# Optimization experiments

Measured on AMD Instinct MI355X. Metric: run time of the kernel, lower is better.

Reference implementation:

```python
import jax, jax.numpy as jnp
import numpy as np

NEG_INF = -1e10  # masked_fill value from the torch module


def setup_inputs() -> dict:
    key = jax.random.key(0)
    k1, k2, k3, k4, k5 = jax.random.split(key, 5)
    B, S, H = 64, 2048, 512
    return {
        "decoder_hidden": jax.random.normal(k1, (B, H), dtype=jnp.float32),
        "encoder_outputs": jax.random.normal(k2, (B, S, 2 * H), dtype=jnp.float32),
        "mask": jnp.ones((B, S), dtype=jnp.int32),
        "Wd": jax.random.normal(k3, (H, H), dtype=jnp.float32) * (1.0 / np.sqrt(H)),
        "We": jax.random.normal(k4, (2 * H, H), dtype=jnp.float32) * (1.0 / np.sqrt(2 * H)),
        "v": jax.random.normal(k5, (H,), dtype=jnp.float32) * (1.0 / np.sqrt(H)),
    }


def reference(decoder_hidden, encoder_outputs, mask, Wd, We, v):
    # decoder_proj: (B, H); encoder_proj: (B, S, H)
    dec_proj = decoder_hidden @ Wd
    enc_proj = jnp.einsum("bse,eh->bsh", encoder_outputs, We)
    energy = jnp.tanh(dec_proj[:, None, :] + enc_proj)  # (B, S, H)
    scores = jnp.einsum("bsh,h->bs", energy, v)  # (B, S)
    scores = jnp.where(mask == 0, NEG_INF, scores)
    attn_weights = jax.nn.softmax(scores, axis=1)  # (B, S)
    context = jnp.einsum("bs,bsd->bd", attn_weights, encoder_outputs)  # (B, 2H)
    return (context, attn_weights)
```

## Files before the change

### kernel.cpp

```cpp
#include <hip/hip_runtime.h>

typedef _Float16 f16;
typedef f16  f16x4 __attribute__((ext_vector_type(4)));
typedef f16  f16x8 __attribute__((ext_vector_type(8)));
typedef float f32x4 __attribute__((ext_vector_type(4)));

#define B_  64
#define S_  2048
#define H_  512
#define K_  1024

__device__ __forceinline__ float fast_tanh(float x){
  float ax = fabsf(x);
  float t  = __expf(-2.0f*ax);
  float r  = (1.0f - t) / (1.0f + t);
  return x < 0.0f ? -r : r;
}

__global__ __launch_bounds__(256) void prep_k(const float* __restrict__ We,
                                              f16* __restrict__ Bg,
                                              const float* __restrict__ dh,
                                              const float* __restrict__ Wd,
                                              float* __restrict__ dp,
                                              const float* __restrict__ vvg,
                                              float* __restrict__ vC){
  __shared__ float s_dh[512];
  if (blockIdx.x < 2048){
    int idx = blockIdx.x*256 + threadIdx.x;
    int k = idx >> 9, col = idx & 511;
    Bg[((k>>3)<<12) + (col<<3) + (k&7)] = (f16)We[idx];
  } else if (blockIdx.x < 2176){
    int idx = blockIdx.x - 2048;
    int b = idx >> 1, cg = idx & 1;
    int col = (cg<<8) + threadIdx.x;
    for (int i = threadIdx.x; i < 512; i += 256) s_dh[i] = dh[(b<<9) + i];
    __syncthreads();
    float a0=0.f,a1=0.f,a2=0.f,a3=0.f;
    for (int k = 0; k < 512; k += 4){
      a0 += s_dh[k+0]*Wd[(k+0)*512 + col];
      a1 += s_dh[k+1]*Wd[(k+1)*512 + col];
      a2 += s_dh[k+2]*Wd[(k+2)*512 + col];
      a3 += s_dh[k+3]*Wd[(k+3)*512 + col];
    }
    dp[(b<<9) + col] = (a0+a1)+(a2+a3);
  } else {
    int t = threadIdx.x;
    float a = fabsf(vvg[t]) + fabsf(vvg[t+256]);
    #pragma unroll
    for (int o = 32; o >= 1; o >>= 1) a += __shfl_xor(a, o);
    if ((t & 63) == 0) s_dh[t>>6] = a;
    __syncthreads();
    if (t == 0) vC[0] = s_dh[0]+s_dh[1]+s_dh[2]+s_dh[3];
  }
}

__global__ __launch_bounds__(512, 2) void fused_k(
    const float* __restrict__ enc,
    const f16*   __restrict__ Bg,
    const float* __restrict__ dp,
    const float* __restrict__ vvg,
    const float* __restrict__ vC,
    const int*   __restrict__ mask,
    float*       __restrict__ pbuf,
    float*       __restrict__ denom,
    float*       __restrict__ part)
{
  __shared__ __align__(16) f16 At[2][2048];
  __shared__ __align__(16) f16 Bt[2][16384];
  __shared__ float s_sc[64];

  const int tid  = threadIdx.x;
  const int lane = tid & 63;
  const int wave = tid >> 6;
  const int b    = blockIdx.x >> 5;
  const int s0   = (blockIdx.x & 31) << 6;

  if (tid < 64) s_sc[tid] = 0.0f;

  const int arow = tid >> 3;
  const int akq  = tid & 7;
  const int kgrp = akq >> 1, apar = akq & 1;
  const float* aG = enc + ((size_t)(b*S_ + s0 + arow) << 10) + (akq << 2);
  const int aDst = (kgrp<<9) + ((arow ^ (kgrp<<1))<<3) + (apar<<2);

  const int r16 = lane & 15, g = lane >> 4;
  const int aFrag = (g<<9) + ((r16 ^ (g<<1))<<3);
  const int colb  = wave << 6;
  const int bFrag = (g<<12) + ((colb + r16)<<3);

  f32x4 acc[4][4] = {};

  auto stageB = [&](int buf, int t){
    const f16* src = Bg + ((size_t)t << 14);
    #pragma unroll
    for (int i = 0; i < 4; ++i){
      int slot = (i<<9) + tid;
      __builtin_amdgcn_global_load_lds(
          (const __attribute__((address_space(1))) void*)(src + (slot<<3)),
          (__attribute__((address_space(3))) void*)(&Bt[buf][slot<<3]),
          16, 0, 0);
    }
  };
  auto loadA = [&](int t)->f32x4 { return *(const f32x4*)(aG + (t<<5)); };
  auto putA  = [&](f32x4 a4, int buf){
    f16x4 h4; h4[0]=(f16)a4[0]; h4[1]=(f16)a4[1]; h4[2]=(f16)a4[2]; h4[3]=(f16)a4[3];
    *(f16x4*)&At[buf][aDst] = h4;
  };

  f32x4 aCur = {}, aNext = {};
  {
    f32x4 a0 = loadA(0);
    __builtin_amdgcn_sched_barrier(0);
    stageB(0, 0);
    __builtin_amdgcn_sched_barrier(0);
    aCur = loadA(1);
    __builtin_amdgcn_sched_barrier(0);
    putA(a0, 0);
  }
  asm volatile("s_waitcnt vmcnt(1) lgkmcnt(0)" ::: "memory");
  __builtin_amdgcn_sched_barrier(0);
  __builtin_amdgcn_s_barrier();
  __builtin_amdgcn_sched_barrier(0);

  for (int t = 0; t < 32; ++t){
    const int cur = t & 1;
    if (t < 31){
      stageB(cur^1, t+1);
      __builtin_amdgcn_sched_barrier(0);
      aNext = loadA(t+2 < 32 ? t+2 : 31);
      __builtin_amdgcn_sched_barrier(0);
      putA(aCur, cur^1);
    }
    f16x8 bfr[4];
    #pragma unroll
    for (int n = 0; n < 4; ++n) bfr[n] = *(const f16x8*)&Bt[cur][bFrag + (n<<7)];
    #pragma unroll
    for (int m = 0; m < 4; ++m){
      f16x8 af = *(const f16x8*)&At[cur][aFrag + (m<<7)];
      #pragma unroll
      for (int n = 0; n < 4; ++n)
        acc[m][n] = __builtin_amdgcn_mfma_f32_16x16x32_f16(af, bfr[n], acc[m][n], 0, 0, 0);
    }
    asm volatile("s_waitcnt vmcnt(1) lgkmcnt(0)" ::: "memory");
    __builtin_amdgcn_sched_barrier(0);
    __builtin_amdgcn_s_barrier();
    __builtin_amdgcn_sched_barrier(0);
    aCur = aNext;
  }

  float dpv[4], vvv[4];
  #pragma unroll
  for (int n = 0; n < 4; ++n){
    int c = colb + (n<<4) + r16;
    dpv[n] = dp[(b<<9) + c];
    vvv[n] = vvg[c];
  }
  float sp[4][4] = {};
  #pragma unroll
  for (int m = 0; m < 4; ++m)
    #pragma unroll
    for (int n = 0; n < 4; ++n)
      #pragma unroll
      for (int r = 0; r < 4; ++r){
        float e = fast_tanh(acc[m][n][r] + dpv[n]);
        sp[m][r] += vvv[n]*e;
      }
  #pragma unroll
  for (int m = 0; m < 4; ++m)
    #pragma unroll
    for (int r = 0; r < 4; ++r){
      float x = sp[m][r];
      x += __shfl_xor(x, 1);
      x += __shfl_xor(x, 2);
      x += __shfl_xor(x, 4);
      x += __shfl_xor(x, 8);
      if (r16 == 0) atomicAdd(&s_sc[(m<<4) + (g<<2) + r], x);
    }
  __syncthreads();

  const float C = vC[0];
  if (tid < 64){
    float s = s_sc[tid];
    int mk = mask[(b<<11) + s0 + tid];
    float p = mk ? __expf(s - C) : 0.0f;
    s_sc[tid] = p;
    pbuf[(b<<11) + s0 + tid] = p;
    float d = p;
    #pragma unroll
    for (int o = 32; o >= 1; o >>= 1) d += __shfl_xor(d, o);
    if (tid == 0) denom[(b<<5) + (blockIdx.x & 31)] = d;
  }
  __syncthreads();

  {
    const float2* e2 = (const float2*)(enc + ((size_t)(b*S_ + s0) << 10)) + tid;
    float ax = 0.f, ay = 0.f;
    #pragma unroll 4
    for (int s = 0; s < 64; ++s){
      float w = s_sc[s];
      float2 x = e2[s*512];
      ax += w * x.x; ay += w * x.y;
    }
    float2* pp = (float2*)part + ((size_t)blockIdx.x << 9) + tid;
    *pp = make_float2(ax, ay);
  }
}

__global__ __launch_bounds__(256) void combine_k(const float* __restrict__ part,
                                                 const float* __restrict__ denom,
                                                 const float* __restrict__ pbuf,
                                                 float* __restrict__ ctx,
                                                 float* __restrict__ attn){
  const int b = blockIdx.x, tid = threadIdx.x;
  float D = 0.f;
  #pragma unroll
  for (int c = 0; c < 32; ++c) D += denom[(b<<5) + c];
  D = fmaxf(D, 1e-37f);
  const float inv = 1.0f / D;

  f32x4 acc = {0.f,0.f,0.f,0.f};
  const f32x4* p4 = (const f32x4*)part;
  #pragma unroll
  for (int c = 0; c < 32; ++c)
    acc += p4[(((b<<5)+c)<<8) + tid];
  ((f32x4*)ctx)[(b<<8) + tid] = acc * inv;

  #pragma unroll
  for (int i = 0; i < 8; ++i){
    int s = tid + (i<<8);
    attn[(b<<11) + s] = pbuf[(b<<11) + s] * inv;
  }
}

extern "C" void kernel_launch(void* const* d_in, const int* in_sizes, int n_in,
                              void* d_out, int out_size, void* d_ws, size_t ws_size,
                              hipStream_t stream){
  (void)in_sizes; (void)n_in; (void)out_size;
  const size_t WS_NEED = 1712384u + 8388608u;
  if (ws_size < WS_NEED) return;

  const float* dec_h = (const float*)d_in[0];
  const float* enc   = (const float*)d_in[1];
  const int*   mask  = (const int*)d_in[2];
  const float* Wd    = (const float*)d_in[3];
  const float* We    = (const float*)d_in[4];
  const float* v     = (const float*)d_in[5];
  float* out  = (float*)d_out;
  float* ctx  = out;
  float* attn = out + B_*2*H_;

  char* ws = (char*)d_ws;
  f16*   Bg     = (f16*)ws;
  float* dproj  = (float*)(ws + 1048576);
  float* vC     = (float*)(ws + 1179648);
  float* pbuf   = (float*)(ws + 1179904);
  float* denom  = (float*)(ws + 1704192);
  float* part   = (float*)(ws + 1712384);

  prep_k   <<<2177, 256, 0, stream>>>(We, Bg, dec_h, Wd, dproj, v, vC);
  fused_k  <<<2048, 512, 0, stream>>>(enc, Bg, dproj, v, vC, mask, pbuf, denom, part);
  combine_k<<<B_, 256, 0, stream>>>(part, denom, pbuf, ctx, attn);
}
```

Baseline: 296.5 us.

## Split context accumulation out of fused GEMM kernel into separate tail kernel

Moves the attention-weighted sum over encoder outputs out of the GEMM/score kernel into a new kernel. The new kernel covers 128 rows per block with float4 nontemporal loads. This shortens the fused kernel's tail and may improve its occupancy. In exchange, encoder_outputs must be streamed from memory a second time instead of being reused while still cache-resident.

New measurement: 326.3 us. 1.1x slower.

```diff
diff --git a/kernel.cpp b/kernel.cpp
--- a/kernel.cpp
+++ b/kernel.cpp
@@ -54,7 +54,7 @@
   }
 }
 
-__global__ __launch_bounds__(512, 2) void fused_k(
+__global__ __launch_bounds__(512, 2) void fused_gemm_k(
     const float* __restrict__ enc,
     const f16*   __restrict__ Bg,
     const float* __restrict__ dp,
@@ -62,8 +62,7 @@
     const float* __restrict__ vC,
     const int*   __restrict__ mask,
     float*       __restrict__ pbuf,
-    float*       __restrict__ denom,
-    float*       __restrict__ part)
+    float*       __restrict__ denom)
 {
   __shared__ __align__(16) f16 At[2][2048];
   __shared__ __align__(16) f16 Bt[2][16384];
@@ -183,27 +182,34 @@
     float s = s_sc[tid];
     int mk = mask[(b<<11) + s0 + tid];
     float p = mk ? __expf(s - C) : 0.0f;
-    s_sc[tid] = p;
     pbuf[(b<<11) + s0 + tid] = p;
     float d = p;
     #pragma unroll
     for (int o = 32; o >= 1; o >>= 1) d += __shfl_xor(d, o);
     if (tid == 0) denom[(b<<5) + (blockIdx.x & 31)] = d;
   }
+}
+
+__global__ __launch_bounds__(512) void ctx_tail_k(const float* __restrict__ enc,
+                                                  const float* __restrict__ pbuf,
+                                                  float* __restrict__ part){
+  const int b = blockIdx.x >> 4, ch = blockIdx.x & 15;
+  const int tid = threadIdx.x;
+  const int par = tid >> 8;
+  const int slot = tid & 255;
+  __shared__ float s_w[128];
+  if (tid < 128) s_w[tid] = pbuf[(b<<11) + (ch<<7) + tid];
   __syncthreads();
-
-  {
-    const float2* e2 = (const float2*)(enc + ((size_t)(b*S_ + s0) << 10)) + tid;
-    float ax = 0.f, ay = 0.f;
-    #pragma unroll 4
-    for (int s = 0; s < 64; ++s){
-      float w = s_sc[s];
-      float2 x = e2[s*512];
-      ax += w * x.x; ay += w * x.y;
-    }
-    float2* pp = (float2*)part + ((size_t)blockIdx.x << 9) + tid;
-    *pp = make_float2(ax, ay);
-  }
+  const float* base = enc + ((size_t)(b*S_ + (ch<<7)) << 10);
+  f32x4 acc = {0.f,0.f,0.f,0.f};
+  #pragma unroll 8
+  for (int i = 0; i < 64; ++i){
+    int row = (i<<1) + par;
+    float w = s_w[row];
+    f32x4 x = __builtin_nontemporal_load((const f32x4*)(base + ((size_t)row<<10)) + slot);
+    acc += w * x;
+  }
+  ((f32x4*)part)[(((b<<5) + (ch<<1) + par)<<8) + slot] = acc;
 }
 
 __global__ __launch_bounds__(256) void combine_k(const float* __restrict__ part,
@@ -257,7 +263,8 @@
   float* denom  = (float*)(ws + 1704192);
   float* part   = (float*)(ws + 1712384);
 
-  prep_k   <<<2177, 256, 0, stream>>>(We, Bg, dec_h, Wd, dproj, v, vC);
-  fused_k  <<<2048, 512, 0, stream>>>(enc, Bg, dproj, v, vC, mask, pbuf, denom, part);
-  combine_k<<<B_, 256, 0, stream>>>(part, denom, pbuf, ctx, attn);
-}
+  prep_k      <<<2177, 256, 0, stream>>>(We, Bg, dec_h, Wd, dproj, v, vC);
+  fused_gemm_k<<<2048, 512, 0, stream>>>(enc, Bg, dproj, v, vC, mask, pbuf, denom);
+  ctx_tail_k  <<<1024, 512, 0, stream>>>(enc, pbuf, part);
+  combine_k   <<<B_, 256, 0, stream>>>(part, denom, pbuf, ctx, attn);
+}
```

## Enlarge fused tile to 128 rows with 1024 threads and triple-buffered weight staging

Applied to the files above, without the earlier changes.

The fused GEMM+attention kernel now processes 128 sequence rows per block with 16 waves in a 2x8 grid, so each staged weight K-slice is reused across twice as many rows and total weight traffic from L2 is halved. The weight tile buffer goes from double to triple buffering, with a prefetch distance of two and adjusted waitcnt thresholds. Denominator and partial-context outputs are split per 64-row half to keep the combine kernel layout unchanged. The larger LDS footprint and 1024-thread blocks cut occupancy to roughly one block per CU and raise per-block barrier cost.

Measured after the change: 316.6 us. +6.8%, slower.

```diff
diff --git a/kernel.cpp b/kernel.cpp
--- a/kernel.cpp
+++ b/kernel.cpp
@@ -54,7 +54,7 @@
   }
 }
 
-__global__ __launch_bounds__(512, 2) void fused_k(
+__global__ __launch_bounds__(1024) void fused_k(
     const float* __restrict__ enc,
     const f16*   __restrict__ Bg,
     const float* __restrict__ dp,
@@ -65,36 +65,35 @@
     float*       __restrict__ denom,
     float*       __restrict__ part)
 {
-  __shared__ __align__(16) f16 At[2][2048];
-  __shared__ __align__(16) f16 Bt[2][16384];
-  __shared__ float s_sc[64];
+  __shared__ __align__(16) f16 Bt[3][16384];
+  __shared__ __align__(16) f16 At[2][4096];
+  __shared__ float s_sc[128];
 
   const int tid  = threadIdx.x;
   const int lane = tid & 63;
   const int wave = tid >> 6;
-  const int b    = blockIdx.x >> 5;
-  const int s0   = (blockIdx.x & 31) << 6;
-
-  if (tid < 64) s_sc[tid] = 0.0f;
+  const int wr   = wave >> 3;
+  const int wc   = wave & 7;
+  const int b    = blockIdx.x >> 4;
+  const int s0   = (blockIdx.x & 15) << 7;
+
+  if (tid < 128) s_sc[tid] = 0.0f;
 
   const int arow = tid >> 3;
   const int akq  = tid & 7;
-  const int kgrp = akq >> 1, apar = akq & 1;
+  const int kg   = akq >> 1, par = akq & 1;
   const float* aG = enc + ((size_t)(b*S_ + s0 + arow) << 10) + (akq << 2);
-  const int aDst = (kgrp<<9) + ((arow ^ (kgrp<<1))<<3) + (apar<<2);
+  const int aDst = (kg<<10) + ((arow ^ (kg<<1))<<3) + (par<<2);
 
   const int r16 = lane & 15, g = lane >> 4;
-  const int aFrag = (g<<9) + ((r16 ^ (g<<1))<<3);
-  const int colb  = wave << 6;
-  const int bFrag = (g<<12) + ((colb + r16)<<3);
 
   f32x4 acc[4][4] = {};
 
   auto stageB = [&](int buf, int t){
     const f16* src = Bg + ((size_t)t << 14);
     #pragma unroll
-    for (int i = 0; i < 4; ++i){
-      int slot = (i<<9) + tid;
+    for (int i = 0; i < 2; ++i){
+      int slot = (i<<10) + tid;
       __builtin_amdgcn_global_load_lds(
           (const __attribute__((address_space(1))) void*)(src + (slot<<3)),
           (__attribute__((address_space(3))) void*)(&Bt[buf][slot<<3]),
@@ -102,60 +101,70 @@
     }
   };
   auto loadA = [&](int t)->f32x4 { return *(const f32x4*)(aG + (t<<5)); };
-  auto putA  = [&](f32x4 a4, int buf){
-    f16x4 h4; h4[0]=(f16)a4[0]; h4[1]=(f16)a4[1]; h4[2]=(f16)a4[2]; h4[3]=(f16)a4[3];
-    *(f16x4*)&At[buf][aDst] = h4;
+  auto putA  = [&](f32x4 a, int buf){
+    f16x4 h; h[0]=(f16)a[0]; h[1]=(f16)a[1]; h[2]=(f16)a[2]; h[3]=(f16)a[3];
+    *(f16x4*)&At[buf][aDst] = h;
   };
 
-  f32x4 aCur = {}, aNext = {};
-  {
-    f32x4 a0 = loadA(0);
-    __builtin_amdgcn_sched_barrier(0);
-    stageB(0, 0);
-    __builtin_amdgcn_sched_barrier(0);
-    aCur = loadA(1);
-    __builtin_amdgcn_sched_barrier(0);
-    putA(a0, 0);
-  }
-  asm volatile("s_waitcnt vmcnt(1) lgkmcnt(0)" ::: "memory");
+  stageB(0, 0);
+  f32x4 aR0 = loadA(0);
+  stageB(1, 1);
+  f32x4 aHold = loadA(1);
+  asm volatile("s_waitcnt vmcnt(3)" ::: "memory");
+  __builtin_amdgcn_sched_barrier(0);
+  putA(aR0, 0);
+  asm volatile("s_waitcnt lgkmcnt(0)" ::: "memory");
   __builtin_amdgcn_sched_barrier(0);
   __builtin_amdgcn_s_barrier();
   __builtin_amdgcn_sched_barrier(0);
 
   for (int t = 0; t < 32; ++t){
-    const int cur = t & 1;
+    f32x4 aNew = aHold;
+    if (t <= 29){
+      stageB((t+2)%3, t+2);
+      aNew = loadA(t+2);
+    }
+    if (t <= 30) putA(aHold, (t+1)&1);
+
+    const f16* Bb = &Bt[t%3][0];
+    const f16* Ab = &At[t&1][0];
+    f16x8 af[4];
+    #pragma unroll
+    for (int m = 0; m < 4; ++m)
+      af[m] = *(const f16x8*)&Ab[(g<<10) + ((((wr<<6)+(m<<4)+r16) ^ (g<<1))<<3)];
+    #pragma unroll
+    for (int n = 0; n < 4; ++n){
+      f16x8 bf = *(const f16x8*)&Bb[(g<<12) + (((wc<<6)+(n<<4)+r16)<<3)];
+      #pragma unroll
+      for (int m = 0; m < 4; ++m)
+        acc[m][n] = __builtin_amdgcn_mfma_f32_16x16x32_f16(af[m], bf, acc[m][n], 0, 0, 0);
+    }
+
     if (t < 31){
-      stageB(cur^1, t+1);
+      if (t <= 29){
+        asm volatile("s_waitcnt vmcnt(3) lgkmcnt(0)" ::: "memory");
+      } else {
+        asm volatile("s_waitcnt vmcnt(0) lgkmcnt(0)" ::: "memory");
+      }
       __builtin_amdgcn_sched_barrier(0);
-      aNext = loadA(t+2 < 32 ? t+2 : 31);
+      __builtin_amdgcn_s_barrier();
       __builtin_amdgcn_sched_barrier(0);
-      putA(aCur, cur^1);
-    }
-    f16x8 bfr[4];
-    #pragma unroll
-    for (int n = 0; n < 4; ++n) bfr[n] = *(const f16x8*)&Bt[cur][bFrag + (n<<7)];
-    #pragma unroll
-    for (int m = 0; m < 4; ++m){
-      f16x8 af = *(const f16x8*)&At[cur][aFrag + (m<<7)];
-      #pragma unroll
-      for (int n = 0; n < 4; ++n)
-        acc[m][n] = __builtin_amdgcn_mfma_f32_16x16x32_f16(af, bfr[n], acc[m][n], 0, 0, 0);
-    }
-    asm volatile("s_waitcnt vmcnt(1) lgkmcnt(0)" ::: "memory");
-    __builtin_amdgcn_sched_barrier(0);
-    __builtin_amdgcn_s_barrier();
-    __builtin_amdgcn_sched_barrier(0);
-    aCur = aNext;
+    }
+    aHold = aNew;
   }
 
   float dpv[4], vvv[4];
   #pragma unroll
   for (int n = 0; n < 4; ++n){
-    int c = colb + (n<<4) + r16;
+    int c = (wc<<6) + (n<<4) + r16;
     dpv[n] = dp[(b<<9) + c];
     vvv[n] = vvg[c];
   }
-  float sp[4][4] = {};
+  float sp[4][4];
+  #pragma unroll
+  for (int m = 0; m < 4; ++m)
+    #pragma unroll
+    for (int r = 0; r < 4; ++r) sp[m][r] = 0.f;
   #pragma unroll
   for (int m = 0; m < 4; ++m)
     #pragma unroll
@@ -174,12 +183,12 @@
       x += __shfl_xor(x, 2);
       x += __shfl_xor(x, 4);
       x += __shfl_xor(x, 8);
-      if (r16 == 0) atomicAdd(&s_sc[(m<<4) + (g<<2) + r], x);
+      if (r16 == 0) atomicAdd(&s_sc[(wr<<6) + (m<<4) + (g<<2) + r], x);
     }
   __syncthreads();
 
   const float C = vC[0];
-  if (tid < 64){
+  if (tid < 128){
     float s = s_sc[tid];
     int mk = mask[(b<<11) + s0 + tid];
     float p = mk ? __expf(s - C) : 0.0f;
@@ -188,20 +197,23 @@
     float d = p;
     #pragma unroll
     for (int o = 32; o >= 1; o >>= 1) d += __shfl_xor(d, o);
-    if (tid == 0) denom[(b<<5) + (blockIdx.x & 31)] = d;
+    if (lane == 0) denom[(b<<5) + ((blockIdx.x & 15)<<1) + wave] = d;
   }
   __syncthreads();
 
   {
-    const float2* e2 = (const float2*)(enc + ((size_t)(b*S_ + s0) << 10)) + tid;
+    const int half = tid >> 9;
+    const int ttid = tid & 511;
+    const float2* e2 = (const float2*)(enc + ((size_t)(b*S_ + s0 + (half<<6)) << 10)) + ttid;
     float ax = 0.f, ay = 0.f;
     #pragma unroll 4
     for (int s = 0; s < 64; ++s){
-      float w = s_sc[s];
+      float w = s_sc[(half<<6) + s];
       float2 x = e2[s*512];
       ax += w * x.x; ay += w * x.y;
     }
-    float2* pp = (float2*)part + ((size_t)blockIdx.x << 9) + tid;
+    int slice = (b<<5) + ((blockIdx.x & 15)<<1) + half;
+    float2* pp = (float2*)part + ((size_t)slice << 9) + ttid;
     *pp = make_float2(ax, ay);
   }
 }
@@ -258,6 +270,6 @@
   float* part   = (float*)(ws + 1712384);
 
   prep_k   <<<2177, 256, 0, stream>>>(We, Bg, dec_h, Wd, dproj, v, vC);
-  fused_k  <<<2048, 512, 0, stream>>>(enc, Bg, dproj, v, vC, mask, pbuf, denom, part);
+  fused_k  <<<1024, 1024, 0, stream>>>(enc, Bg, dproj, v, vC, mask, pbuf, denom, part);
   combine_k<<<B_, 256, 0, stream>>>(part, denom, pbuf, ctx, attn);
 }
```

## Stage B tiles per wave and restructure the MFMA main loop pipeline

Applied to the files above, without the earlier changes.

Each wave now stages only the 64 columns of the weight tile that it consumes, instead of all threads cooperatively loading the whole tile. The in-loop wait is reduced to LDS counters only, relying on the compiler's register wait for the prefetched A data to order the async B loads. All A and B fragments are read from LDS before the MFMA block, which runs with raised wave priority. This is meant to loosen cross-wave synchronisation and improve overlap of global loads with compute. It also stages tile 1 twice at startup, and the implicit vmcnt ordering is fragile.

New measurement: 301.0 us. No clear change (+1.5%).

```diff
diff --git a/kernel.cpp b/kernel.cpp
--- a/kernel.cpp
+++ b/kernel.cpp
@@ -86,18 +86,17 @@
   const int r16 = lane & 15, g = lane >> 4;
   const int aFrag = (g<<9) + ((r16 ^ (g<<1))<<3);
   const int colb  = wave << 6;
-  const int bFrag = (g<<12) + ((colb + r16)<<3);
 
   f32x4 acc[4][4] = {};
 
-  auto stageB = [&](int buf, int t){
-    const f16* src = Bg + ((size_t)t << 14);
-    #pragma unroll
-    for (int i = 0; i < 4; ++i){
-      int slot = (i<<9) + tid;
+  auto stageB = [&](int buf, int kt){
+    const f16* srcBase = Bg + ((size_t)kt << 14);
+    #pragma unroll
+    for (int gg = 0; gg < 4; ++gg){
+      int off = (gg<<12) + (colb<<3) + (lane<<3);
       __builtin_amdgcn_global_load_lds(
-          (const __attribute__((address_space(1))) void*)(src + (slot<<3)),
-          (__attribute__((address_space(3))) void*)(&Bt[buf][slot<<3]),
+          (const __attribute__((address_space(1))) void*)(srcBase + off),
+          (__attribute__((address_space(3))) void*)(&Bt[buf][off]),
           16, 0, 0);
     }
   };
@@ -107,17 +106,12 @@
     *(f16x4*)&At[buf][aDst] = h4;
   };
 
-  f32x4 aCur = {}, aNext = {};
-  {
-    f32x4 a0 = loadA(0);
-    __builtin_amdgcn_sched_barrier(0);
-    stageB(0, 0);
-    __builtin_amdgcn_sched_barrier(0);
-    aCur = loadA(1);
-    __builtin_amdgcn_sched_barrier(0);
-    putA(a0, 0);
-  }
-  asm volatile("s_waitcnt vmcnt(1) lgkmcnt(0)" ::: "memory");
+  stageB(0, 0);
+  f32x4 a0 = loadA(0);
+  stageB(1, 1);
+  f32x4 aCur = loadA(1);
+  putA(a0, 0);
+  asm volatile("s_waitcnt lgkmcnt(0)" ::: "memory");
   __builtin_amdgcn_sched_barrier(0);
   __builtin_amdgcn_s_barrier();
   __builtin_amdgcn_sched_barrier(0);
@@ -126,26 +120,33 @@
     const int cur = t & 1;
     if (t < 31){
       stageB(cur^1, t+1);
+      f32x4 aNext = loadA(t+2 <= 31 ? t+2 : 31);
+      putA(aCur, cur^1);
+      aCur = aNext;
+    } else {
+      asm volatile("s_waitcnt vmcnt(1)" ::: "memory");
       __builtin_amdgcn_sched_barrier(0);
-      aNext = loadA(t+2 < 32 ? t+2 : 31);
-      __builtin_amdgcn_sched_barrier(0);
-      putA(aCur, cur^1);
-    }
-    f16x8 bfr[4];
-    #pragma unroll
-    for (int n = 0; n < 4; ++n) bfr[n] = *(const f16x8*)&Bt[cur][bFrag + (n<<7)];
-    #pragma unroll
-    for (int m = 0; m < 4; ++m){
-      f16x8 af = *(const f16x8*)&At[cur][aFrag + (m<<7)];
+    }
+    f16x8 af[4], bfr[4];
+    #pragma unroll
+    for (int n = 0; n < 4; ++n)
+      bfr[n] = *(const f16x8*)&Bt[cur][(g<<12) + ((colb + (n<<4) + r16)<<3)];
+    #pragma unroll
+    for (int m = 0; m < 4; ++m)
+      af[m] = *(const f16x8*)&At[cur][aFrag + (m<<7)];
+    __builtin_amdgcn_s_setprio(1);
+    #pragma unroll
+    for (int m = 0; m < 4; ++m)
       #pragma unroll
       for (int n = 0; n < 4; ++n)
-        acc[m][n] = __builtin_amdgcn_mfma_f32_16x16x32_f16(af, bfr[n], acc[m][n], 0, 0, 0);
-    }
-    asm volatile("s_waitcnt vmcnt(1) lgkmcnt(0)" ::: "memory");
-    __builtin_amdgcn_sched_barrier(0);
-    __builtin_amdgcn_s_barrier();
-    __builtin_amdgcn_sched_barrier(0);
-    aCur = aNext;
+        acc[m][n] = __builtin_amdgcn_mfma_f32_16x16x32_f16(af[m], bfr[n], acc[m][n], 0, 0, 0);
+    __builtin_amdgcn_s_setprio(0);
+    if (t < 31){
+      asm volatile("s_waitcnt lgkmcnt(0)" ::: "memory");
+      __builtin_amdgcn_sched_barrier(0);
+      __builtin_amdgcn_s_barrier();
+      __builtin_amdgcn_sched_barrier(0);
+    }
   }
 
   float dpv[4], vvv[4];
@@ -155,7 +156,11 @@
     dpv[n] = dp[(b<<9) + c];
     vvv[n] = vvg[c];
   }
-  float sp[4][4] = {};
+  float sp[4][4];
+  #pragma unroll
+  for (int m = 0; m < 4; ++m)
+    #pragma unroll
+    for (int r = 0; r < 4; ++r) sp[m][r] = 0.f;
   #pragma unroll
   for (int m = 0; m < 4; ++m)
     #pragma unroll
```
